# Performance work log

Measured on AMD Instinct MI355X. Metric: run time of the kernel, lower is better.

The kernel has to match this reference:

```python
import jax, jax.numpy as jnp
import numpy as np

N_NODES = 100000
N_EDGES = 1250000
D_IN = 64
D_OUT = 64


def setup_inputs() -> dict:
    key = jax.random.key(0)
    k1, k2, k3, k4, k5, k6 = jax.random.split(key, 6)
    x = jax.random.normal(k1, (N_NODES, D_IN), dtype=jnp.float32)
    W_self = jax.random.normal(k2, (D_IN, D_OUT), dtype=jnp.float32) / np.sqrt(D_IN)
    W_neigh = jax.random.normal(k3, (D_IN, D_OUT), dtype=jnp.float32) / np.sqrt(D_IN)
    b = jax.random.normal(k4, (D_OUT,), dtype=jnp.float32) * 0.01
    src = jax.random.randint(k5, (N_EDGES,), 0, N_NODES, dtype=jnp.int32)
    dst = jnp.sort(jax.random.randint(k6, (N_EDGES,), 0, N_NODES, dtype=jnp.int32))
    return {"x": x, "W_self": W_self, "W_neigh": W_neigh, "b": b, "src": src, "dst": dst}


def reference(x, W_self, W_neigh, b, src, dst):
    # DGL SAGEConv (aggregator_type='mean'):
    #   h_neigh[v] = mean_{u in N(v)} x[u]   (0 if in-degree 0)
    #   out = x @ W_self + h_neigh @ W_neigh + b
    n_nodes = x.shape[0]
    msgs = x[src]  # [E, D_IN] gather of source features
    agg = jax.ops.segment_sum(msgs, dst, num_segments=n_nodes)  # [N, D_IN]
    deg = jax.ops.segment_sum(jnp.ones_like(dst, dtype=x.dtype), dst, num_segments=n_nodes)
    h_neigh = agg / jnp.maximum(deg, 1.0)[:, None]
    return x @ W_self + h_neigh @ W_neigh + b
```

## Files before the change

kernel.cpp:

```cpp
#include <hip/hip_runtime.h>
#include <hip/hip_fp16.h>

#define NN 100000
#define NE 1250000
#define D 64
#define MT 6250
#define RP_BLOCKS 4883
#define ANB 8
#define MAXLE 2048

typedef _Float16 h8 __attribute__((ext_vector_type(8)));
typedef float f4 __attribute__((ext_vector_type(4)));

__device__ inline float2 cvt2(unsigned u) {
    __half2 h = __builtin_bit_cast(__half2, u);
    return __half22float2(h);
}

__global__ __launch_bounds__(256) void k_prep(const int* __restrict__ dst,
                                              int* __restrict__ row_ptr,
                                              const float* __restrict__ Ws,
                                              const float* __restrict__ Wn,
                                              __half* __restrict__ Wp) {
    if (blockIdx.x < RP_BLOCKS) {
        const int i = blockIdx.x * 256 + threadIdx.x;
        if (i >= NE) return;
        const int d = dst[i];
        const int prev = (i == 0) ? -1 : dst[i - 1];
        for (int v = prev + 1; v <= d; ++v) row_ptr[v] = i;
        if (i == NE - 1) {
            for (int v = d + 1; v <= NN; ++v) row_ptr[v] = NE;
        }
    } else {
        const int id = (blockIdx.x - RP_BLOCKS) * 256 + threadIdx.x;
        const int p = id >> 13;
        const int r = id & 8191;
        const int i = r & 7;
        const int l = (r >> 3) & 63;
        const int f = (r >> 9) & 1;
        const int t = r >> 10;
        const int k = f * 32 + ((l >> 4) * 8) + i;
        const int c = (t & 3) * 16 + (l & 15);
        const float v = ((t < 4) ? Ws : Wn)[k * D + c];
        const _Float16 hi = (_Float16)v;
        const _Float16 out = p ? (_Float16)(v - (float)hi) : hi;
        Wp[p * 8192 + r] = __builtin_bit_cast(__half, out);
    }
}

__global__ __launch_bounds__(256) void k_mm(const float* __restrict__ x,
                                            const __half* __restrict__ Wp,
                                            const float* __restrict__ b,
                                            float* __restrict__ z,
                                            __half* __restrict__ y) {
    const int lane = threadIdx.x & 63;
    const int mt = blockIdx.x * 4 + (threadIdx.x >> 6);
    if (mt >= MT) return;
    const int row = lane & 15;
    const int kg = lane >> 4;
    const float* __restrict__ xr = x + (size_t)(mt * 16 + row) * D + kg * 8;

    const float4 v0 = *(const float4*)(xr);
    const float4 v1 = *(const float4*)(xr + 4);
    const float4 v2 = *(const float4*)(xr + 32);
    const float4 v3 = *(const float4*)(xr + 36);

    const float xf0[8] = {v0.x, v0.y, v0.z, v0.w, v1.x, v1.y, v1.z, v1.w};
    const float xf1[8] = {v2.x, v2.y, v2.z, v2.w, v3.x, v3.y, v3.z, v3.w};
    h8 ah0, al0, ah1, al1;
    #pragma unroll
    for (int i = 0; i < 8; ++i) {
        const _Float16 h0 = (_Float16)xf0[i];
        ah0[i] = h0;
        al0[i] = (_Float16)(xf0[i] - (float)h0);
        const _Float16 h1 = (_Float16)xf1[i];
        ah1[i] = h1;
        al1[i] = (_Float16)(xf1[i] - (float)h1);
    }

    const _Float16* __restrict__ wp = (const _Float16*)Wp;
    #pragma unroll
    for (int t = 0; t < 8; ++t) {
        const h8 bh0 = *(const h8*)(wp + ((t * 2 + 0) * 64 + lane) * 8);
        const h8 bh1 = *(const h8*)(wp + ((t * 2 + 1) * 64 + lane) * 8);
        const h8 bl0 = *(const h8*)(wp + 8192 + ((t * 2 + 0) * 64 + lane) * 8);
        const h8 bl1 = *(const h8*)(wp + 8192 + ((t * 2 + 1) * 64 + lane) * 8);
        f4 acc = {0.f, 0.f, 0.f, 0.f};
        acc = __builtin_amdgcn_mfma_f32_16x16x32_f16(al0, bh0, acc, 0, 0, 0);
        acc = __builtin_amdgcn_mfma_f32_16x16x32_f16(al1, bh1, acc, 0, 0, 0);
        acc = __builtin_amdgcn_mfma_f32_16x16x32_f16(ah0, bl0, acc, 0, 0, 0);
        acc = __builtin_amdgcn_mfma_f32_16x16x32_f16(ah1, bl1, acc, 0, 0, 0);
        acc = __builtin_amdgcn_mfma_f32_16x16x32_f16(ah0, bh0, acc, 0, 0, 0);
        acc = __builtin_amdgcn_mfma_f32_16x16x32_f16(ah1, bh1, acc, 0, 0, 0);

        const int col = (t & 3) * 16 + (lane & 15);
        const int r0 = mt * 16 + kg * 4;
        if (t < 4) {
            const float bb = b[col];
            #pragma unroll
            for (int reg = 0; reg < 4; ++reg)
                z[(size_t)(r0 + reg) * D + col] = acc[reg] + bb;
        } else {
            #pragma unroll
            for (int reg = 0; reg < 4; ++reg)
                y[(size_t)(r0 + reg) * D + col] = __float2half(acc[reg]);
        }
    }
}

__global__ __launch_bounds__(256) void k_aggr(const __half* __restrict__ y,
                                              const int* __restrict__ src,
                                              const int* __restrict__ row_ptr,
                                              float* __restrict__ out) {
    __shared__ int s_src[MAXLE];
    __shared__ int s_rp[ANB + 1];
    const int tid = threadIdx.x;
    const int v0 = blockIdx.x * ANB;

    if (tid <= ANB) s_rp[tid] = row_ptr[v0 + tid];
    __syncthreads();
    const int base = s_rp[0];
    const int cnt = s_rp[ANB] - base;
    const bool fits = (cnt <= MAXLE);
    if (fits) {
        for (int i = tid; i < cnt; i += 256) s_src[i] = src[base + i];
    }
    __syncthreads();

    const int lane = tid & 63;
    const int half = lane >> 5;
    const int w    = lane & 31;
    const int node = (tid >> 6) * 2 + half;
    const int v    = v0 + node;
    const int lo = s_rp[node];
    const int hi = s_rp[node + 1];
    const int deg = hi - lo;

    float a0 = 0.0f, a1 = 0.0f;
    if (deg > 0) {
        const int last = hi - 1;
        if (fits) {
            for (int e = lo; e < hi; e += 8) {
                int sv[8];
                #pragma unroll
                for (int u = 0; u < 8; ++u)
                    sv[u] = s_src[min(e + u, last) - base];
                unsigned r[8];
                #pragma unroll
                for (int u = 0; u < 8; ++u)
                    r[u] = *(const unsigned*)(y + (size_t)sv[u] * D + w * 2);
                #pragma unroll
                for (int u = 0; u < 8; ++u) {
                    if (e + u < hi) {
                        const float2 f = cvt2(r[u]);
                        a0 += f.x; a1 += f.y;
                    }
                }
            }
        } else {
            for (int e = lo; e < hi; e += 8) {
                int sv[8];
                #pragma unroll
                for (int u = 0; u < 8; ++u) sv[u] = src[min(e + u, last)];
                unsigned r[8];
                #pragma unroll
                for (int u = 0; u < 8; ++u)
                    r[u] = *(const unsigned*)(y + (size_t)sv[u] * D + w * 2);
                #pragma unroll
                for (int u = 0; u < 8; ++u) {
                    if (e + u < hi) {
                        const float2 f = cvt2(r[u]);
                        a0 += f.x; a1 += f.y;
                    }
                }
            }
        }
    }
    const float inv = (deg > 0) ? 1.0f / (float)deg : 0.0f;
    float2* op = (float2*)(out + (size_t)v * D + w * 2);
    float2 o = *op;
    o.x += a0 * inv;
    o.y += a1 * inv;
    *op = o;
}

extern "C" void kernel_launch(void* const* d_in, const int* in_sizes, int n_in,
                              void* d_out, int out_size, void* d_ws, size_t ws_size,
                              hipStream_t stream) {
    const float* x      = (const float*)d_in[0];
    const float* Wself  = (const float*)d_in[1];
    const float* Wneigh = (const float*)d_in[2];
    const float* b      = (const float*)d_in[3];
    const int*   src    = (const int*)d_in[4];
    const int*   dst    = (const int*)d_in[5];
    float* out = (float*)d_out;

    __half* y = (__half*)d_ws;
    const size_t yb = (size_t)NN * D * 2;
    int* row_ptr = (int*)((char*)d_ws + yb);
    const size_t rpb = (((size_t)(NN + 1) * 4) + 15) & ~(size_t)15;
    __half* Wp = (__half*)((char*)d_ws + yb + rpb);

    k_prep<<<RP_BLOCKS + 64, 256, 0, stream>>>(dst, row_ptr, Wself, Wneigh, Wp);
    k_mm<<<(MT + 3) / 4, 256, 0, stream>>>(x, Wp, b, out, y);
    k_aggr<<<NN / ANB, 256, 0, stream>>>(y, src, row_ptr, out);
}
```

Measured before the change: 133.0 us.

## Slice projected neighbor features into column strips for cache-local gather

The fp16 projected neighbor features are now stored as four column slices of 16 halves each (32 bytes per node per slice) instead of one 128-byte row. The aggregation grid is split so consecutive blocks handle the same 32 nodes but different slices, with 8 threads per node gathering one slice. The goal is to shrink each slice's working set so it stays resident in cache during the random gather. In exchange, each source-index list is read four times, and each gathered row segment is 32 bytes, which may waste memory sectors.

```diff
diff --git a/kernel.cpp b/kernel.cpp
--- a/kernel.cpp
+++ b/kernel.cpp
@@ -6,7 +6,8 @@
 #define D 64
 #define MT 6250
 #define RP_BLOCKS 4883
-#define ANB 8
+#define ANB 32
+#define NSL 4
 #define MAXLE 2048
 
 typedef _Float16 h8 __attribute__((ext_vector_type(8)));
@@ -52,7 +53,7 @@
                                             const __half* __restrict__ Wp,
                                             const float* __restrict__ b,
                                             float* __restrict__ z,
-                                            __half* __restrict__ y) {
+                                            __half* __restrict__ yt) {
     const int lane = threadIdx.x & 63;
     const int mt = blockIdx.x * 4 + (threadIdx.x >> 6);
     if (mt >= MT) return;
@@ -93,29 +94,32 @@
         acc = __builtin_amdgcn_mfma_f32_16x16x32_f16(ah0, bh0, acc, 0, 0, 0);
         acc = __builtin_amdgcn_mfma_f32_16x16x32_f16(ah1, bh1, acc, 0, 0, 0);
 
-        const int col = (t & 3) * 16 + (lane & 15);
         const int r0 = mt * 16 + kg * 4;
         if (t < 4) {
+            const int col = (t & 3) * 16 + (lane & 15);
             const float bb = b[col];
             #pragma unroll
             for (int reg = 0; reg < 4; ++reg)
                 z[(size_t)(r0 + reg) * D + col] = acc[reg] + bb;
         } else {
+            const int s = t & 3;
             #pragma unroll
             for (int reg = 0; reg < 4; ++reg)
-                y[(size_t)(r0 + reg) * D + col] = __float2half(acc[reg]);
+                yt[((size_t)s * NN + r0 + reg) * 16 + (lane & 15)] =
+                    __float2half(acc[reg]);
         }
     }
 }
 
-__global__ __launch_bounds__(256) void k_aggr(const __half* __restrict__ y,
+__global__ __launch_bounds__(256) void k_aggr(const __half* __restrict__ yt,
                                               const int* __restrict__ src,
                                               const int* __restrict__ row_ptr,
                                               float* __restrict__ out) {
     __shared__ int s_src[MAXLE];
     __shared__ int s_rp[ANB + 1];
     const int tid = threadIdx.x;
-    const int v0 = blockIdx.x * ANB;
+    const int s  = blockIdx.x & (NSL - 1);
+    const int v0 = (blockIdx.x >> 2) * ANB;
 
     if (tid <= ANB) s_rp[tid] = row_ptr[v0 + tid];
     __syncthreads();
@@ -127,28 +131,26 @@
     }
     __syncthreads();
 
-    const int lane = tid & 63;
-    const int half = lane >> 5;
-    const int w    = lane & 31;
-    const int node = (tid >> 6) * 2 + half;
+    const int node = tid >> 3;
+    const int q    = tid & 7;
     const int v    = v0 + node;
     const int lo = s_rp[node];
     const int hi = s_rp[node + 1];
     const int deg = hi - lo;
+
+    const unsigned* __restrict__ yrow = (const unsigned*)yt + (size_t)s * NN * 8 + q;
 
     float a0 = 0.0f, a1 = 0.0f;
     if (deg > 0) {
         const int last = hi - 1;
         if (fits) {
             for (int e = lo; e < hi; e += 8) {
-                int sv[8];
-                #pragma unroll
-                for (int u = 0; u < 8; ++u)
-                    sv[u] = s_src[min(e + u, last) - base];
                 unsigned r[8];
                 #pragma unroll
-                for (int u = 0; u < 8; ++u)
-                    r[u] = *(const unsigned*)(y + (size_t)sv[u] * D + w * 2);
+                for (int u = 0; u < 8; ++u) {
+                    const int sv = s_src[min(e + u, last) - base];
+                    r[u] = yrow[(size_t)sv * 8];
+                }
                 #pragma unroll
                 for (int u = 0; u < 8; ++u) {
                     if (e + u < hi) {
@@ -159,13 +161,12 @@
             }
         } else {
             for (int e = lo; e < hi; e += 8) {
-                int sv[8];
-                #pragma unroll
-                for (int u = 0; u < 8; ++u) sv[u] = src[min(e + u, last)];
                 unsigned r[8];
                 #pragma unroll
-                for (int u = 0; u < 8; ++u)
-                    r[u] = *(const unsigned*)(y + (size_t)sv[u] * D + w * 2);
+                for (int u = 0; u < 8; ++u) {
+                    const int sv = src[min(e + u, last)];
+                    r[u] = yrow[(size_t)sv * 8];
+                }
                 #pragma unroll
                 for (int u = 0; u < 8; ++u) {
                     if (e + u < hi) {
@@ -177,7 +178,7 @@
         }
     }
     const float inv = (deg > 0) ? 1.0f / (float)deg : 0.0f;
-    float2* op = (float2*)(out + (size_t)v * D + w * 2);
+    float2* op = (float2*)(out + (size_t)v * D + s * 16 + q * 2);
     float2 o = *op;
     o.x += a0 * inv;
     o.y += a1 * inv;
@@ -195,13 +196,13 @@
     const int*   dst    = (const int*)d_in[5];
     float* out = (float*)d_out;
 
-    __half* y = (__half*)d_ws;
+    __half* yt = (__half*)d_ws;
     const size_t yb = (size_t)NN * D * 2;
     int* row_ptr = (int*)((char*)d_ws + yb);
     const size_t rpb = (((size_t)(NN + 1) * 4) + 15) & ~(size_t)15;
     __half* Wp = (__half*)((char*)d_ws + yb + rpb);
 
     k_prep<<<RP_BLOCKS + 64, 256, 0, stream>>>(dst, row_ptr, Wself, Wneigh, Wp);
-    k_mm<<<(MT + 3) / 4, 256, 0, stream>>>(x, Wp, b, out, y);
-    k_aggr<<<NN / ANB, 256, 0, stream>>>(y, src, row_ptr, out);
-}
+    k_mm<<<(MT + 3) / 4, 256, 0, stream>>>(x, Wp, b, out, yt);
+    k_aggr<<<(NN / ANB) * NSL, 256, 0, stream>>>(yt, src, row_ptr, out);
+}
```

After: 147.1 us. 10.5% more time.
